# Performance work log

Measured on AMD Instinct MI355X. Metric: run time of the kernel, lower is better.

Reference implementation:

```python
import jax, jax.numpy as jnp
import numpy as np

N = 50000   # nodes
E = 800000  # edges
F_IN, H, C, G = 128, 96, 16, 128  # features, hidden, classes, graphs


def gelu(x):
    return jax.nn.gelu(x, approximate=False)  # torch F.gelu default (erf)


def gcn_conv(x, W, b, src, dst, dis):
    # PyG GCNConv improved=True: A_hat = A + 2I, out = D^-1/2 A_hat D^-1/2 (x W) + b
    xw = x @ W                                   # [N, out]
    norm = dis[src] * dis[dst]                   # [E]
    msg = norm[:, None] * xw[src]                # gather + scale
    out = jax.ops.segment_sum(msg, dst, num_segments=N)
    out = out + (2.0 * dis * dis)[:, None] * xw  # self-loop with weight 2
    return out + b


def setup_inputs() -> dict:
    key = jax.random.key(0)
    ks = jax.random.split(key, 12)
    x = jax.random.normal(ks[0], (N, F_IN), dtype=jnp.float32)
    edge_index = jax.random.randint(ks[1], (2, E), 0, N, dtype=jnp.int64)
    batch = jnp.sort(jax.random.randint(ks[2], (N,), 0, G, dtype=jnp.int64))
    s = lambda fan_in: 1.0 / np.sqrt(fan_in)
    W0 = jax.random.uniform(ks[3], (F_IN, H), jnp.float32, -s(F_IN), s(F_IN))
    b0 = jnp.zeros((H,), jnp.float32)
    W1 = jax.random.uniform(ks[4], (H, H), jnp.float32, -s(H), s(H))
    b1 = jnp.zeros((H,), jnp.float32)
    W2 = jax.random.uniform(ks[5], (H, H), jnp.float32, -s(H), s(H))
    b2 = jnp.zeros((H,), jnp.float32)
    Wc1 = jax.random.uniform(ks[6], (2 * H, H), jnp.float32, -s(2 * H), s(2 * H))
    bc1 = jax.random.uniform(ks[7], (H,), jnp.float32, -s(2 * H), s(2 * H))
    Wc2 = jax.random.uniform(ks[8], (H, C), jnp.float32, -s(H), s(H))
    bc2 = jax.random.uniform(ks[9], (C,), jnp.float32, -s(H), s(H))
    return {"x": x, "edge_index": edge_index, "batch": batch,
            "W0": W0, "b0": b0, "W1": W1, "b1": b1, "W2": W2, "b2": b2,
            "Wc1": Wc1, "bc1": bc1, "Wc2": Wc2, "bc2": bc2}


def reference(x, edge_index, batch, W0, b0, W1, b1, W2, b2, Wc1, bc1, Wc2, bc2):
    src, dst = edge_index[0], edge_index[1]
    # degrees including self-loop weight 2 (improved=True)
    deg = jax.ops.segment_sum(jnp.ones((E,), x.dtype), dst, num_segments=N) + 2.0
    dis = jax.lax.rsqrt(deg)
    # layer 0: GCNConv(F_IN -> H)
    h = gcn_conv(x, W0, b0, src, dst, dis)
    # residual GCNConv layers (dropout is identity at inference)
    h = h + gcn_conv(gelu(h), W1, b1, src, dst, dis)
    h = h + gcn_conv(gelu(h), W2, b2, src, dst, dis)
    h = gelu(h)
    # global mean + max pooling per graph
    cnt = jax.ops.segment_sum(jnp.ones((N,), h.dtype), batch, num_segments=G)
    mean_p = jax.ops.segment_sum(h, batch, num_segments=G) / cnt[:, None]
    max_p = jax.ops.segment_max(h, batch, num_segments=G)
    p = jnp.concatenate([mean_p, max_p], axis=1)  # [G, 2H]
    p = p @ Wc1 + bc1
    p = gelu(p)
    return p @ Wc2 + bc2
```

## Files before the change

### kernel.cpp

```cpp
#include <hip/hip_runtime.h>
#include <hip/hip_bf16.h>

#define DEVINL __device__ __forceinline__

constexpr int N = 50000;
constexpr int E = 800000;
constexpr int F_IN = 128;
constexpr int H = 96;
constexpr int C = 16;
constexpr int G = 128;
constexpr int S = 8;
constexpr int ELLW = 64;

constexpr int OFF_W0  = 0;
constexpr int OFF_W1  = OFF_W0 + F_IN * H;
constexpr int OFF_W2  = OFF_W1 + H * H;
constexpr int OFF_WC1 = OFF_W2 + H * H;
constexpr int OFF_WC2 = OFF_WC1 + 2 * H * H;
constexpr int OFF_B0  = OFF_WC2 + H * C;
constexpr int OFF_B1  = OFF_B0 + H;
constexpr int OFF_B2  = OFF_B1 + H;
constexpr int OFF_BC1 = OFF_B2 + H;
constexpr int OFF_BC2 = OFF_BC1 + H;
constexpr int WF_TOT  = OFF_BC2 + C;

constexpr int CVB   = (WF_TOT + 255) / 256;
constexpr int GEMB  = (N + 31) / 32;
constexpr int SCATB = (E / 2 + 127) / 128;

DEVINL float gelu_f(float x) {
    return 0.5f * x * (1.0f + erff(x * 0.70710678118654752440f));
}

DEVINL int detect_eidx_i64(const int* e) {
    int z = 0;
#pragma unroll
    for (int i = 1; i < 16; i += 2) z |= e[i];
    return z == 0;
}
DEVINL int detect_batch_i64(const int* a) {
    int z = 0;
    for (int i = 20001; i < 20032; i += 2) z |= a[i];
    return z == 0;
}
DEVINL int detect_x_f32(const unsigned short* xu) {
    int bad = 0;
    for (int i = 0; i < 128; i += 2) { int ex = (xu[i] >> 7) & 0xFF; if (ex >= 132) bad = 1; }
    return bad;
}

DEVINL unsigned pk(float a, float b) {
    __hip_bfloat16 ha = __float2bfloat16(a), hb = __float2bfloat16(b);
    unsigned short ua = *(unsigned short*)&ha, ub = *(unsigned short*)&hb;
    return (unsigned)ua | ((unsigned)ub << 16);
}
DEVINL float lo16(unsigned u) { return __uint_as_float(u << 16); }
DEVINL float hi16(unsigned u) { return __uint_as_float(u & 0xffff0000u); }

DEVINL float disv(int c) { return rsqrtf((float)c + 2.0f); }

__global__ void k_prep(const void* W0, const void* W1, const void* W2,
                       const void* Wc1, const void* Wc2,
                       const void* b0, const void* b1, const void* b2,
                       const void* bc1, const void* bc2,
                       const void* x, float* __restrict__ wf, int* __restrict__ cnt) {
    int i = blockIdx.x * 256 + threadIdx.x;
    if (i < N) cnt[i] = 0;
    if (i >= WF_TOT) return;
    int f32 = detect_x_f32((const unsigned short*)x);
    const void* src; int j;
    if      (i < OFF_W1)  { src = W0;  j = i - OFF_W0; }
    else if (i < OFF_W2)  { src = W1;  j = i - OFF_W1; }
    else if (i < OFF_WC1) { src = W2;  j = i - OFF_W2; }
    else if (i < OFF_WC2) { src = Wc1; j = i - OFF_WC1; }
    else if (i < OFF_B0)  { src = Wc2; j = i - OFF_WC2; }
    else if (i < OFF_B1)  { src = b0;  j = i - OFF_B0; }
    else if (i < OFF_B2)  { src = b1;  j = i - OFF_B1; }
    else if (i < OFF_BC1) { src = b2;  j = i - OFF_B2; }
    else if (i < OFF_BC2) { src = bc1; j = i - OFF_BC1; }
    else                  { src = bc2; j = i - OFF_BC2; }
    wf[i] = f32 ? ((const float*)src)[j]
                : __bfloat162float(((const __hip_bfloat16*)src)[j]);
}

template<int K, int KC, bool RAW_IN, bool GELU_IN, bool SCALE_OUT>
DEVINL void gemm_tile(const void* __restrict__ inp, const float* __restrict__ Wf,
                      const int* __restrict__ cnt,
                      int xf32, unsigned* __restrict__ out, int bid, int t) {
    constexpr int R = 32;
    constexpr int NC = K / KC;
    __shared__ __align__(16) float xs[KC][R + 4];
    __shared__ __align__(16) float wsh[KC * 96];
    const int r0 = bid * R;
    const int ty = t >> 4;
    const int tx = t & 15;

    float acc[4][6];
#pragma unroll
    for (int i = 0; i < 4; ++i)
#pragma unroll
        for (int j = 0; j < 6; ++j) acc[i][j] = 0.f;

    for (int c = 0; c < NC; ++c) {
        if (c) __syncthreads();
        for (int idx = t * 4; idx < KC * 96; idx += 128 * 4)
            *(float4*)&wsh[idx] = *(const float4*)&Wf[c * KC * 96 + idx];
        if (RAW_IN && !xf32) {
            for (int idx = t; idx < R * KC; idx += 128) {
                int r = idx / KC, kk = idx - r * KC;
                int row = r0 + r, k = c * KC + kk;
                float v = 0.f;
                if (row < N) v = __bfloat162float(((const __hip_bfloat16*)inp)[(size_t)row * K + k]);
                xs[kk][r] = v;
            }
        } else {
            constexpr int KC4 = KC / 4;
            for (int idx = t; idx < R * KC4; idx += 128) {
                int r = idx / KC4, k4 = (idx - r * KC4) * 4;
                int row = r0 + r, k = c * KC + k4;
                float4 v = make_float4(0.f, 0.f, 0.f, 0.f);
                if (row < N) v = *(const float4*)((const float*)inp + (size_t)row * K + k);
                if (GELU_IN) { v.x = gelu_f(v.x); v.y = gelu_f(v.y); v.z = gelu_f(v.z); v.w = gelu_f(v.w); }
                xs[k4 + 0][r] = v.x; xs[k4 + 1][r] = v.y; xs[k4 + 2][r] = v.z; xs[k4 + 3][r] = v.w;
            }
        }
        __syncthreads();

#pragma unroll 4
        for (int kk = 0; kk < KC; ++kk) {
            float4 av = *(const float4*)&xs[kk][ty * 4];
            float2 b0 = *(const float2*)&wsh[kk * 96 + tx * 6];
            float2 b1 = *(const float2*)&wsh[kk * 96 + tx * 6 + 2];
            float2 b2 = *(const float2*)&wsh[kk * 96 + tx * 6 + 4];
            float a[4] = {av.x, av.y, av.z, av.w};
            float b[6] = {b0.x, b0.y, b1.x, b1.y, b2.x, b2.y};
#pragma unroll
            for (int i = 0; i < 4; ++i)
#pragma unroll
                for (int j = 0; j < 6; ++j)
                    acc[i][j] = fmaf(a[i], b[j], acc[i][j]);
        }
    }

#pragma unroll
    for (int i = 0; i < 4; ++i) {
        int row = r0 + ty * 4 + i;
        if (row < N) {
            float d = SCALE_OUT ? disv(cnt[row]) : 1.0f;
            unsigned* o = out + (size_t)row * 48 + tx * 3;
            o[0] = pk(d * acc[i][0], d * acc[i][1]);
            o[1] = pk(d * acc[i][2], d * acc[i][3]);
            o[2] = pk(d * acc[i][4], d * acc[i][5]);
        }
    }
}

__global__ __launch_bounds__(128) void k_sg(const void* __restrict__ x,
                                            const float* __restrict__ Wf,
                                            const int* __restrict__ eidx,
                                            int* __restrict__ cnt, int* __restrict__ ell,
                                            unsigned* __restrict__ outZ) {
    int b = blockIdx.x, t = threadIdx.x;
    if (b % 3 == 0) {
        int gb = b / 3;
        if (gb >= GEMB) return;
        int xf32 = detect_x_f32((const unsigned short*)x);
        gemm_tile<F_IN, 32, true, false, false>(x, Wf, nullptr, xf32, outZ, gb, t);
        return;
    }
    int sb = (b / 3) * 2 + (b % 3) - 1;
    if (sb >= SCATB) return;
    int t2 = sb * 128 + t;
    int e = 2 * t2;
    if (e >= E) return;
    int i64 = detect_eidx_i64(eidx);
    int s0, s1, d0, d1;
    if (i64) {
        int4 sp = *(const int4*)(eidx + 4 * t2);
        int4 dp = *(const int4*)(eidx + 2 * E + 4 * t2);
        s0 = sp.x; s1 = sp.z; d0 = dp.x; d1 = dp.z;
    } else {
        int2 sp = *(const int2*)(eidx + 2 * t2);
        int2 dp = *(const int2*)(eidx + E + 2 * t2);
        s0 = sp.x; s1 = sp.y; d0 = dp.x; d1 = dp.y;
    }
    int p0 = atomicAdd(&cnt[d0], 1);
    if (p0 < ELLW) ell[d0 * ELLW + p0] = s0;
    if (e + 1 < E) {
        int p1 = atomicAdd(&cnt[d1], 1);
        if (p1 < ELLW) ell[d1 * ELLW + p1] = s1;
    }
}

template<int K, int KC, bool GELU_IN>
__global__ __launch_bounds__(128) void k_gemm(const float* __restrict__ inp,
                                              const float* __restrict__ Wf,
                                              const int* __restrict__ cnt,
                                              unsigned* __restrict__ out) {
    gemm_tile<K, KC, false, GELU_IN, true>(inp, Wf, cnt, 1, out, blockIdx.x, threadIdx.x);
}

template<bool PRESCALED>
__global__ __launch_bounds__(256) void k_aggr(const unsigned* __restrict__ xw, const float* res,
                                              const int* __restrict__ ell, const int* __restrict__ cnt,
                                              const float* __restrict__ bias, float* __restrict__ out) {
    __shared__ int   sIdx[4][ELLW];
    __shared__ float sW[4][ELLW];
    int wid = threadIdx.x >> 6, lane = threadIdx.x & 63;
    int n = blockIdx.x * 4 + wid;
    if (n >= N) return;
    int cn = cnt[n];
    int cc = min(cn, ELLW);
    if (lane < cc) {
        int idx = ell[n * ELLW + lane];
        sIdx[wid][lane] = idx;
        if (!PRESCALED) sW[wid][lane] = disv(cnt[idx]);
    }
    int slot = lane / 12;
    int li = lane - slot * 12;
    int cp = li * 4;
    float4 A0 = make_float4(0.f, 0.f, 0.f, 0.f);
    float4 A1 = make_float4(0.f, 0.f, 0.f, 0.f);
    int j = (slot < 5) ? slot : cc;
    for (; j + 10 < cc; j += 15) {
        int s0 = sIdx[wid][j];
        int s1 = sIdx[wid][j + 5];
        int s2 = sIdx[wid][j + 10];
        uint4 u0 = *(const uint4*)(xw + (size_t)s0 * 48 + cp);
        uint4 u1 = *(const uint4*)(xw + (size_t)s1 * 48 + cp);
        uint4 u2 = *(const uint4*)(xw + (size_t)s2 * 48 + cp);
        if (PRESCALED) {
            A0.x += lo16(u0.x) + lo16(u1.x) + lo16(u2.x);
            A0.y += hi16(u0.x) + hi16(u1.x) + hi16(u2.x);
            A0.z += lo16(u0.y) + lo16(u1.y) + lo16(u2.y);
            A0.w += hi16(u0.y) + hi16(u1.y) + hi16(u2.y);
            A1.x += lo16(u0.z) + lo16(u1.z) + lo16(u2.z);
            A1.y += hi16(u0.z) + hi16(u1.z) + hi16(u2.z);
            A1.z += lo16(u0.w) + lo16(u1.w) + lo16(u2.w);
            A1.w += hi16(u0.w) + hi16(u1.w) + hi16(u2.w);
        } else {
            float w0 = sW[wid][j];
            float w1 = sW[wid][j + 5];
            float w2 = sW[wid][j + 10];
            A0.x = fmaf(w0, lo16(u0.x), A0.x); A0.y = fmaf(w0, hi16(u0.x), A0.y);
            A0.z = fmaf(w0, lo16(u0.y), A0.z); A0.w = fmaf(w0, hi16(u0.y), A0.w);
            A1.x = fmaf(w0, lo16(u0.z), A1.x); A1.y = fmaf(w0, hi16(u0.z), A1.y);
            A1.z = fmaf(w0, lo16(u0.w), A1.z); A1.w = fmaf(w0, hi16(u0.w), A1.w);
            A0.x = fmaf(w1, lo16(u1.x), A0.x); A0.y = fmaf(w1, hi16(u1.x), A0.y);
            A0.z = fmaf(w1, lo16(u1.y), A0.z); A0.w = fmaf(w1, hi16(u1.y), A0.w);
            A1.x = fmaf(w1, lo16(u1.z), A1.x); A1.y = fmaf(w1, hi16(u1.z), A1.y);
            A1.z = fmaf(w1, lo16(u1.w), A1.z); A1.w = fmaf(w1, hi16(u1.w), A1.w);
            A0.x = fmaf(w2, lo16(u2.x), A0.x); A0.y = fmaf(w2, hi16(u2.x), A0.y);
            A0.z = fmaf(w2, lo16(u2.y), A0.z); A0.w = fmaf(w2, hi16(u2.y), A0.w);
            A1.x = fmaf(w2, lo16(u2.z), A1.x); A1.y = fmaf(w2, hi16(u2.z), A1.y);
            A1.z = fmaf(w2, lo16(u2.w), A1.z); A1.w = fmaf(w2, hi16(u2.w), A1.w);
        }
    }
    for (; j < cc; j += 5) {
        int s = sIdx[wid][j];
        uint4 u = *(const uint4*)(xw + (size_t)s * 48 + cp);
        if (PRESCALED) {
            A0.x += lo16(u.x); A0.y += hi16(u.x); A0.z += lo16(u.y); A0.w += hi16(u.y);
            A1.x += lo16(u.z); A1.y += hi16(u.z); A1.z += lo16(u.w); A1.w += hi16(u.w);
        } else {
            float w = sW[wid][j];
            A0.x = fmaf(w, lo16(u.x), A0.x); A0.y = fmaf(w, hi16(u.x), A0.y);
            A0.z = fmaf(w, lo16(u.y), A0.z); A0.w = fmaf(w, hi16(u.y), A0.w);
            A1.x = fmaf(w, lo16(u.z), A1.x); A1.y = fmaf(w, hi16(u.z), A1.y);
            A1.z = fmaf(w, lo16(u.w), A1.z); A1.w = fmaf(w, hi16(u.w), A1.w);
        }
    }
    {
        float g0, g1, g2, g3;
        g0 = __shfl(A0.x, lane + 12); g1 = __shfl(A0.x, lane + 24); g2 = __shfl(A0.x, lane + 36); g3 = __shfl(A0.x, lane + 48);
        A0.x += g0 + g1 + g2 + g3;
        g0 = __shfl(A0.y, lane + 12); g1 = __shfl(A0.y, lane + 24); g2 = __shfl(A0.y, lane + 36); g3 = __shfl(A0.y, lane + 48);
        A0.y += g0 + g1 + g2 + g3;
        g0 = __shfl(A0.z, lane + 12); g1 = __shfl(A0.z, lane + 24); g2 = __shfl(A0.z, lane + 36); g3 = __shfl(A0.z, lane + 48);
        A0.z += g0 + g1 + g2 + g3;
        g0 = __shfl(A0.w, lane + 12); g1 = __shfl(A0.w, lane + 24); g2 = __shfl(A0.w, lane + 36); g3 = __shfl(A0.w, lane + 48);
        A0.w += g0 + g1 + g2 + g3;
        g0 = __shfl(A1.x, lane + 12); g1 = __shfl(A1.x, lane + 24); g2 = __shfl(A1.x, lane + 36); g3 = __shfl(A1.x, lane + 48);
        A1.x += g0 + g1 + g2 + g3;
        g0 = __shfl(A1.y, lane + 12); g1 = __shfl(A1.y, lane + 24); g2 = __shfl(A1.y, lane + 36); g3 = __shfl(A1.y, lane + 48);
        A1.y += g0 + g1 + g2 + g3;
        g0 = __shfl(A1.z, lane + 12); g1 = __shfl(A1.z, lane + 24); g2 = __shfl(A1.z, lane + 36); g3 = __shfl(A1.z, lane + 48);
        A1.z += g0 + g1 + g2 + g3;
        g0 = __shfl(A1.w, lane + 12); g1 = __shfl(A1.w, lane + 24); g2 = __shfl(A1.w, lane + 36); g3 = __shfl(A1.w, lane + 48);
        A1.w += g0 + g1 + g2 + g3;
    }

    if (lane < 12) {
        float dn = disv(cn);
        float sc = PRESCALED ? (2.f * dn) : (2.f * dn * dn);
        int cl = li * 8;
        uint4 su = *(const uint4*)(xw + (size_t)n * 48 + cp);
        float4 sv0 = make_float4(lo16(su.x), hi16(su.x), lo16(su.y), hi16(su.y));
        float4 sv1 = make_float4(lo16(su.z), hi16(su.z), lo16(su.w), hi16(su.w));
        float4 bv0 = *(const float4*)(bias + cl);
        float4 bv1 = *(const float4*)(bias + cl + 4);
        float4 rv0 = make_float4(0.f, 0.f, 0.f, 0.f);
        float4 rv1 = make_float4(0.f, 0.f, 0.f, 0.f);
        if (res) {
            rv0 = *(const float4*)(res + (size_t)n * 96 + cl);
            rv1 = *(const float4*)(res + (size_t)n * 96 + cl + 4);
        }
        float4 o0, o1;
        o0.x = rv0.x + dn * A0.x + sc * sv0.x + bv0.x;
        o0.y = rv0.y + dn * A0.y + sc * sv0.y + bv0.y;
        o0.z = rv0.z + dn * A0.z + sc * sv0.z + bv0.z;
        o0.w = rv0.w + dn * A0.w + sc * sv0.w + bv0.w;
        o1.x = rv1.x + dn * A1.x + sc * sv1.x + bv1.x;
        o1.y = rv1.y + dn * A1.y + sc * sv1.y + bv1.y;
        o1.z = rv1.z + dn * A1.z + sc * sv1.z + bv1.z;
        o1.w = rv1.w + dn * A1.w + sc * sv1.w + bv1.w;
        *(float4*)(out + (size_t)n * 96 + cl) = o0;
        *(float4*)(out + (size_t)n * 96 + cl + 4) = o1;
    }
}

DEVINL int ld_idx(const int* a, int i64, int i) { return i64 ? a[2 * i] : a[i]; }

DEVINL int lbound_s(const int* a, int i64, int n, int key) {
    int lo = 0, hi = n;
    while (lo < hi) { int m = (lo + hi) >> 1; if (ld_idx(a, i64, m) < key) lo = m + 1; else hi = m; }
    return lo;
}

__global__ __launch_bounds__(128) void k_pool(const float* __restrict__ h, const int* __restrict__ batch,
                                              float* __restrict__ part) {
    int i64 = detect_batch_i64(batch);
    int g = blockIdx.x / S, sch = blockIdx.x % S;
    int lo = lbound_s(batch, i64, N, g), hi = lbound_s(batch, i64, N, g + 1);
    int len = hi - lo;
    int a = lo + (int)(((long long)len * sch) / S);
    int b = lo + (int)(((long long)len * (sch + 1)) / S);
    int t = threadIdx.x;
    if (t < 96) {
        float s0 = 0.f, s1 = 0.f, m0 = -INFINITY, m1 = -INFINITY;
        int n = a;
        for (; n + 1 < b; n += 2) {
            float v0 = gelu_f(h[(size_t)n * 96 + t]);
            float v1 = gelu_f(h[(size_t)(n + 1) * 96 + t]);
            s0 += v0; s1 += v1;
            m0 = fmaxf(m0, v0); m1 = fmaxf(m1, v1);
        }
        if (n < b) {
            float v = gelu_f(h[(size_t)n * 96 + t]);
            s0 += v; m0 = fmaxf(m0, v);
        }
        part[(size_t)blockIdx.x * 192 + t] = s0 + s1;
        part[(size_t)blockIdx.x * 192 + 96 + t] = fmaxf(m0, m1);
    }
}

__global__ __launch_bounds__(128) void k_cls(const float* __restrict__ part, const int* __restrict__ batch,
                                             const void* __restrict__ x,
                                             const float* __restrict__ wf, void* __restrict__ outp) {
    __shared__ float p[192];
    __shared__ float q[96];
    int i64 = detect_batch_i64(batch);
    int g = blockIdx.x, t = threadIdx.x;
    int lo = lbound_s(batch, i64, N, g), hi = lbound_s(batch, i64, N, g + 1);
    float inv = (hi > lo) ? 1.f / (float)(hi - lo) : 0.f;
    if (t < 96) {
        float sum = 0.f, mx = -INFINITY;
        for (int s = 0; s < S; ++s) {
            sum += part[(size_t)(g * S + s) * 192 + t];
            mx = fmaxf(mx, part[(size_t)(g * S + s) * 192 + 96 + t]);
        }
        p[t] = sum * inv;
        p[96 + t] = mx;
    }
    __syncthreads();
    if (t < 96) {
        float acc = wf[OFF_BC1 + t];
        const float* Wc1 = wf + OFF_WC1;
        for (int j = 0; j < 192; ++j)
            acc += p[j] * Wc1[j * 96 + t];
        q[t] = gelu_f(acc);
    }
    __syncthreads();
    if (t < 16) {
        float acc = wf[OFF_BC2 + t];
        const float* Wc2 = wf + OFF_WC2;
        for (int j = 0; j < 96; ++j)
            acc += q[j] * Wc2[j * 16 + t];
        if (detect_x_f32((const unsigned short*)x)) ((float*)outp)[g * 16 + t] = acc;
        else ((__hip_bfloat16*)outp)[g * 16 + t] = __float2bfloat16(acc);
    }
}

extern "C" void kernel_launch(void* const* d_in, const int* in_sizes, int n_in,
                              void* d_out, int out_size, void* d_ws, size_t ws_size,
                              hipStream_t stream) {
    const void* x    = d_in[0];
    const int* eidx  = (const int*)d_in[1];
    const int* batch = (const int*)d_in[2];
    (void)in_sizes; (void)n_in; (void)out_size; (void)ws_size;

    char* w = (char*)d_ws;
    size_t off = 0;
    auto take = [&](size_t bytes) { size_t o = off; off += (bytes + 511) & ~(size_t)511; return o; };
    int*      cnt  = (int*)     (w + take((size_t)N * 4));
    float*    wf   = (float*)   (w + take((size_t)WF_TOT * 4));
    int*      ell  = (int*)     (w + take((size_t)N * ELLW * 4));
    unsigned* bufA = (unsigned*)(w + take((size_t)N * 48 * 4));
    float*    bufH = (float*)   (w + take((size_t)N * 96 * 4));
    float*    part = (float*)   (w + take((size_t)G * S * 192 * 4));

    k_prep<<<CVB, 256, 0, stream>>>(d_in[3], d_in[5], d_in[7], d_in[9], d_in[11],
                                    d_in[4], d_in[6], d_in[8], d_in[10], d_in[12],
                                    x, wf, cnt);
    k_sg<<<3 * GEMB, 128, 0, stream>>>(x, wf + OFF_W0, eidx, cnt, ell, bufA);

    int aggr_grid = (N + 3) / 4;
    k_aggr<false><<<aggr_grid, 256, 0, stream>>>(bufA, nullptr, ell, cnt, wf + OFF_B0, bufH);
    k_gemm<H, 48, true><<<GEMB, 128, 0, stream>>>(bufH, wf + OFF_W1, cnt, bufA);
    k_aggr<true><<<aggr_grid, 256, 0, stream>>>(bufA, bufH, ell, cnt, wf + OFF_B1, bufH);
    k_gemm<H, 48, true><<<GEMB, 128, 0, stream>>>(bufH, wf + OFF_W2, cnt, bufA);
    k_aggr<true><<<aggr_grid, 256, 0, stream>>>(bufA, bufH, ell, cnt, wf + OFF_B2, bufH);

    k_pool<<<G * S, 128, 0, stream>>>(bufH, batch, part);
    k_cls<<<G, 128, 0, stream>>>(part, batch, x, wf, d_out);
}
```

Measured before the change: 354.7 us.

## Fuse next-layer GELU+GEMM into aggregation kernel epilogue

The separate GEMM kernels are removed. Each aggregation block now handles 32 nodes and, in its epilogue, applies GELU to the new hidden rows, multiplies them by the next layer's 96x96 weight held in shared memory, and writes the prescaled bf16 features. This drops two kernel launches and the re-read of the hidden buffer from global memory. In exchange every block reloads the 36KB weight matrix, shared memory per block rises (occupancy may drop), and double-buffered xw arrays are needed so a layer does not overwrite its own gather source.

```diff
diff --git a/kernel.cpp b/kernel.cpp
--- a/kernel.cpp
+++ b/kernel.cpp
@@ -27,6 +27,7 @@
 constexpr int CVB   = (WF_TOT + 255) / 256;
 constexpr int GEMB  = (N + 31) / 32;
 constexpr int SCATB = (E / 2 + 127) / 128;
+constexpr int AGB   = (N + 31) / 32;
 
 DEVINL float gelu_f(float x) {
     return 0.5f * x * (1.0f + erff(x * 0.70710678118654752440f));
@@ -192,130 +193,172 @@
     }
 }
 
-template<int K, int KC, bool GELU_IN>
-__global__ __launch_bounds__(128) void k_gemm(const float* __restrict__ inp,
-                                              const float* __restrict__ Wf,
-                                              const int* __restrict__ cnt,
-                                              unsigned* __restrict__ out) {
-    gemm_tile<K, KC, false, GELU_IN, true>(inp, Wf, cnt, 1, out, blockIdx.x, threadIdx.x);
-}
-
-template<bool PRESCALED>
-__global__ __launch_bounds__(256) void k_aggr(const unsigned* __restrict__ xw, const float* res,
-                                              const int* __restrict__ ell, const int* __restrict__ cnt,
-                                              const float* __restrict__ bias, float* __restrict__ out) {
-    __shared__ int   sIdx[4][ELLW];
-    __shared__ float sW[4][ELLW];
-    int wid = threadIdx.x >> 6, lane = threadIdx.x & 63;
-    int n = blockIdx.x * 4 + wid;
-    if (n >= N) return;
-    int cn = cnt[n];
-    int cc = min(cn, ELLW);
-    if (lane < cc) {
-        int idx = ell[n * ELLW + lane];
-        sIdx[wid][lane] = idx;
-        if (!PRESCALED) sW[wid][lane] = disv(cnt[idx]);
-    }
+template<bool PRESCALED, bool EPI>
+__global__ __launch_bounds__(512) void k_ag(const unsigned* __restrict__ xw, const float* res,
+                                            const int* __restrict__ ell, const int* __restrict__ cnt,
+                                            const float* __restrict__ bias,
+                                            const float* __restrict__ Wepi,
+                                            float* __restrict__ outH,
+                                            unsigned* __restrict__ outA) {
+    __shared__ int   sIdx[8][ELLW];
+    __shared__ float sW[8][ELLW];
+    __shared__ float hs[EPI ? 32 : 1][97];
+    __shared__ __align__(16) float wsh[EPI ? 96 * 96 : 4];
+    int t = threadIdx.x;
+    int wv = t >> 6, lane = t & 63;
+    int bn0 = blockIdx.x * 32;
+
+    if (EPI) {
+        for (int idx = t * 4; idx < 96 * 96; idx += 512 * 4)
+            *(float4*)&wsh[idx] = *(const float4*)&Wepi[idx];
+    }
+
     int slot = lane / 12;
     int li = lane - slot * 12;
     int cp = li * 4;
-    float4 A0 = make_float4(0.f, 0.f, 0.f, 0.f);
-    float4 A1 = make_float4(0.f, 0.f, 0.f, 0.f);
-    int j = (slot < 5) ? slot : cc;
-    for (; j + 10 < cc; j += 15) {
-        int s0 = sIdx[wid][j];
-        int s1 = sIdx[wid][j + 5];
-        int s2 = sIdx[wid][j + 10];
-        uint4 u0 = *(const uint4*)(xw + (size_t)s0 * 48 + cp);
-        uint4 u1 = *(const uint4*)(xw + (size_t)s1 * 48 + cp);
-        uint4 u2 = *(const uint4*)(xw + (size_t)s2 * 48 + cp);
-        if (PRESCALED) {
-            A0.x += lo16(u0.x) + lo16(u1.x) + lo16(u2.x);
-            A0.y += hi16(u0.x) + hi16(u1.x) + hi16(u2.x);
-            A0.z += lo16(u0.y) + lo16(u1.y) + lo16(u2.y);
-            A0.w += hi16(u0.y) + hi16(u1.y) + hi16(u2.y);
-            A1.x += lo16(u0.z) + lo16(u1.z) + lo16(u2.z);
-            A1.y += hi16(u0.z) + hi16(u1.z) + hi16(u2.z);
-            A1.z += lo16(u0.w) + lo16(u1.w) + lo16(u2.w);
-            A1.w += hi16(u0.w) + hi16(u1.w) + hi16(u2.w);
-        } else {
-            float w0 = sW[wid][j];
-            float w1 = sW[wid][j + 5];
-            float w2 = sW[wid][j + 10];
-            A0.x = fmaf(w0, lo16(u0.x), A0.x); A0.y = fmaf(w0, hi16(u0.x), A0.y);
-            A0.z = fmaf(w0, lo16(u0.y), A0.z); A0.w = fmaf(w0, hi16(u0.y), A0.w);
-            A1.x = fmaf(w0, lo16(u0.z), A1.x); A1.y = fmaf(w0, hi16(u0.z), A1.y);
-            A1.z = fmaf(w0, lo16(u0.w), A1.z); A1.w = fmaf(w0, hi16(u0.w), A1.w);
-            A0.x = fmaf(w1, lo16(u1.x), A0.x); A0.y = fmaf(w1, hi16(u1.x), A0.y);
-            A0.z = fmaf(w1, lo16(u1.y), A0.z); A0.w = fmaf(w1, hi16(u1.y), A0.w);
-            A1.x = fmaf(w1, lo16(u1.z), A1.x); A1.y = fmaf(w1, hi16(u1.z), A1.y);
-            A1.z = fmaf(w1, lo16(u1.w), A1.z); A1.w = fmaf(w1, hi16(u1.w), A1.w);
-            A0.x = fmaf(w2, lo16(u2.x), A0.x); A0.y = fmaf(w2, hi16(u2.x), A0.y);
-            A0.z = fmaf(w2, lo16(u2.y), A0.z); A0.w = fmaf(w2, hi16(u2.y), A0.w);
-            A1.x = fmaf(w2, lo16(u2.z), A1.x); A1.y = fmaf(w2, hi16(u2.z), A1.y);
-            A1.z = fmaf(w2, lo16(u2.w), A1.z); A1.w = fmaf(w2, hi16(u2.w), A1.w);
-        }
-    }
-    for (; j < cc; j += 5) {
-        int s = sIdx[wid][j];
-        uint4 u = *(const uint4*)(xw + (size_t)s * 48 + cp);
-        if (PRESCALED) {
-            A0.x += lo16(u.x); A0.y += hi16(u.x); A0.z += lo16(u.y); A0.w += hi16(u.y);
-            A1.x += lo16(u.z); A1.y += hi16(u.z); A1.z += lo16(u.w); A1.w += hi16(u.w);
-        } else {
-            float w = sW[wid][j];
-            A0.x = fmaf(w, lo16(u.x), A0.x); A0.y = fmaf(w, hi16(u.x), A0.y);
-            A0.z = fmaf(w, lo16(u.y), A0.z); A0.w = fmaf(w, hi16(u.y), A0.w);
-            A1.x = fmaf(w, lo16(u.z), A1.x); A1.y = fmaf(w, hi16(u.z), A1.y);
-            A1.z = fmaf(w, lo16(u.w), A1.z); A1.w = fmaf(w, hi16(u.w), A1.w);
-        }
-    }
-    {
-        float g0, g1, g2, g3;
-        g0 = __shfl(A0.x, lane + 12); g1 = __shfl(A0.x, lane + 24); g2 = __shfl(A0.x, lane + 36); g3 = __shfl(A0.x, lane + 48);
-        A0.x += g0 + g1 + g2 + g3;
-        g0 = __shfl(A0.y, lane + 12); g1 = __shfl(A0.y, lane + 24); g2 = __shfl(A0.y, lane + 36); g3 = __shfl(A0.y, lane + 48);
-        A0.y += g0 + g1 + g2 + g3;
-        g0 = __shfl(A0.z, lane + 12); g1 = __shfl(A0.z, lane + 24); g2 = __shfl(A0.z, lane + 36); g3 = __shfl(A0.z, lane + 48);
-        A0.z += g0 + g1 + g2 + g3;
-        g0 = __shfl(A0.w, lane + 12); g1 = __shfl(A0.w, lane + 24); g2 = __shfl(A0.w, lane + 36); g3 = __shfl(A0.w, lane + 48);
-        A0.w += g0 + g1 + g2 + g3;
-        g0 = __shfl(A1.x, lane + 12); g1 = __shfl(A1.x, lane + 24); g2 = __shfl(A1.x, lane + 36); g3 = __shfl(A1.x, lane + 48);
-        A1.x += g0 + g1 + g2 + g3;
-        g0 = __shfl(A1.y, lane + 12); g1 = __shfl(A1.y, lane + 24); g2 = __shfl(A1.y, lane + 36); g3 = __shfl(A1.y, lane + 48);
-        A1.y += g0 + g1 + g2 + g3;
-        g0 = __shfl(A1.z, lane + 12); g1 = __shfl(A1.z, lane + 24); g2 = __shfl(A1.z, lane + 36); g3 = __shfl(A1.z, lane + 48);
-        A1.z += g0 + g1 + g2 + g3;
-        g0 = __shfl(A1.w, lane + 12); g1 = __shfl(A1.w, lane + 24); g2 = __shfl(A1.w, lane + 36); g3 = __shfl(A1.w, lane + 48);
-        A1.w += g0 + g1 + g2 + g3;
-    }
-
-    if (lane < 12) {
-        float dn = disv(cn);
-        float sc = PRESCALED ? (2.f * dn) : (2.f * dn * dn);
-        int cl = li * 8;
-        uint4 su = *(const uint4*)(xw + (size_t)n * 48 + cp);
-        float4 sv0 = make_float4(lo16(su.x), hi16(su.x), lo16(su.y), hi16(su.y));
-        float4 sv1 = make_float4(lo16(su.z), hi16(su.z), lo16(su.w), hi16(su.w));
-        float4 bv0 = *(const float4*)(bias + cl);
-        float4 bv1 = *(const float4*)(bias + cl + 4);
-        float4 rv0 = make_float4(0.f, 0.f, 0.f, 0.f);
-        float4 rv1 = make_float4(0.f, 0.f, 0.f, 0.f);
-        if (res) {
-            rv0 = *(const float4*)(res + (size_t)n * 96 + cl);
-            rv1 = *(const float4*)(res + (size_t)n * 96 + cl + 4);
-        }
-        float4 o0, o1;
-        o0.x = rv0.x + dn * A0.x + sc * sv0.x + bv0.x;
-        o0.y = rv0.y + dn * A0.y + sc * sv0.y + bv0.y;
-        o0.z = rv0.z + dn * A0.z + sc * sv0.z + bv0.z;
-        o0.w = rv0.w + dn * A0.w + sc * sv0.w + bv0.w;
-        o1.x = rv1.x + dn * A1.x + sc * sv1.x + bv1.x;
-        o1.y = rv1.y + dn * A1.y + sc * sv1.y + bv1.y;
-        o1.z = rv1.z + dn * A1.z + sc * sv1.z + bv1.z;
-        o1.w = rv1.w + dn * A1.w + sc * sv1.w + bv1.w;
-        *(float4*)(out + (size_t)n * 96 + cl) = o0;
-        *(float4*)(out + (size_t)n * 96 + cl + 4) = o1;
+    int cl = li * 8;
+
+    for (int k = 0; k < 4; ++k) {
+        int r = wv * 4 + k;
+        int n = bn0 + r;
+        if (n >= N) {
+            if (EPI && lane < 12)
+#pragma unroll
+                for (int q = 0; q < 8; ++q) hs[r][cl + q] = 0.f;
+            continue;
+        }
+        int cn = cnt[n];
+        int cc = min(cn, ELLW);
+        if (lane < cc) {
+            int idx = ell[n * ELLW + lane];
+            sIdx[wv][lane] = idx;
+            if (!PRESCALED) sW[wv][lane] = disv(cnt[idx]);
+        }
+        float4 A0 = make_float4(0.f, 0.f, 0.f, 0.f);
+        float4 A1 = make_float4(0.f, 0.f, 0.f, 0.f);
+        int j = (slot < 5) ? slot : cc;
+        for (; j + 10 < cc; j += 15) {
+            int s0 = sIdx[wv][j];
+            int s1 = sIdx[wv][j + 5];
+            int s2 = sIdx[wv][j + 10];
+            uint4 u0 = *(const uint4*)(xw + (size_t)s0 * 48 + cp);
+            uint4 u1 = *(const uint4*)(xw + (size_t)s1 * 48 + cp);
+            uint4 u2 = *(const uint4*)(xw + (size_t)s2 * 48 + cp);
+            if (PRESCALED) {
+                A0.x += lo16(u0.x) + lo16(u1.x) + lo16(u2.x);
+                A0.y += hi16(u0.x) + hi16(u1.x) + hi16(u2.x);
+                A0.z += lo16(u0.y) + lo16(u1.y) + lo16(u2.y);
+                A0.w += hi16(u0.y) + hi16(u1.y) + hi16(u2.y);
+                A1.x += lo16(u0.z) + lo16(u1.z) + lo16(u2.z);
+                A1.y += hi16(u0.z) + hi16(u1.z) + hi16(u2.z);
+                A1.z += lo16(u0.w) + lo16(u1.w) + lo16(u2.w);
+                A1.w += hi16(u0.w) + hi16(u1.w) + hi16(u2.w);
+            } else {
+                float w0 = sW[wv][j];
+                float w1 = sW[wv][j + 5];
+                float w2 = sW[wv][j + 10];
+                A0.x = fmaf(w0, lo16(u0.x), A0.x); A0.y = fmaf(w0, hi16(u0.x), A0.y);
+                A0.z = fmaf(w0, lo16(u0.y), A0.z); A0.w = fmaf(w0, hi16(u0.y), A0.w);
+                A1.x = fmaf(w0, lo16(u0.z), A1.x); A1.y = fmaf(w0, hi16(u0.z), A1.y);
+                A1.z = fmaf(w0, lo16(u0.w), A1.z); A1.w = fmaf(w0, hi16(u0.w), A1.w);
+                A0.x = fmaf(w1, lo16(u1.x), A0.x); A0.y = fmaf(w1, hi16(u1.x), A0.y);
+                A0.z = fmaf(w1, lo16(u1.y), A0.z); A0.w = fmaf(w1, hi16(u1.y), A0.w);
+                A1.x = fmaf(w1, lo16(u1.z), A1.x); A1.y = fmaf(w1, hi16(u1.z), A1.y);
+                A1.z = fmaf(w1, lo16(u1.w), A1.z); A1.w = fmaf(w1, hi16(u1.w), A1.w);
+                A0.x = fmaf(w2, lo16(u2.x), A0.x); A0.y = fmaf(w2, hi16(u2.x), A0.y);
+                A0.z = fmaf(w2, lo16(u2.y), A0.z); A0.w = fmaf(w2, hi16(u2.y), A0.w);
+                A1.x = fmaf(w2, lo16(u2.z), A1.x); A1.y = fmaf(w2, hi16(u2.z), A1.y);
+                A1.z = fmaf(w2, lo16(u2.w), A1.z); A1.w = fmaf(w2, hi16(u2.w), A1.w);
+            }
+        }
+        for (; j < cc; j += 5) {
+            int s = sIdx[wv][j];
+            uint4 u = *(const uint4*)(xw + (size_t)s * 48 + cp);
+            if (PRESCALED) {
+                A0.x += lo16(u.x); A0.y += hi16(u.x); A0.z += lo16(u.y); A0.w += hi16(u.y);
+                A1.x += lo16(u.z); A1.y += hi16(u.z); A1.z += lo16(u.w); A1.w += hi16(u.w);
+            } else {
+                float w = sW[wv][j];
+                A0.x = fmaf(w, lo16(u.x), A0.x); A0.y = fmaf(w, hi16(u.x), A0.y);
+                A0.z = fmaf(w, lo16(u.y), A0.z); A0.w = fmaf(w, hi16(u.y), A0.w);
+                A1.x = fmaf(w, lo16(u.z), A1.x); A1.y = fmaf(w, hi16(u.z), A1.y);
+                A1.z = fmaf(w, lo16(u.w), A1.z); A1.w = fmaf(w, hi16(u.w), A1.w);
+            }
+        }
+        {
+            float g0, g1, g2, g3;
+            g0 = __shfl(A0.x, lane + 12); g1 = __shfl(A0.x, lane + 24); g2 = __shfl(A0.x, lane + 36); g3 = __shfl(A0.x, lane + 48);
+            A0.x += g0 + g1 + g2 + g3;
+            g0 = __shfl(A0.y, lane + 12); g1 = __shfl(A0.y, lane + 24); g2 = __shfl(A0.y, lane + 36); g3 = __shfl(A0.y, lane + 48);
+            A0.y += g0 + g1 + g2 + g3;
+            g0 = __shfl(A0.z, lane + 12); g1 = __shfl(A0.z, lane + 24); g2 = __shfl(A0.z, lane + 36); g3 = __shfl(A0.z, lane + 48);
+            A0.z += g0 + g1 + g2 + g3;
+            g0 = __shfl(A0.w, lane + 12); g1 = __shfl(A0.w, lane + 24); g2 = __shfl(A0.w, lane + 36); g3 = __shfl(A0.w, lane + 48);
+            A0.w += g0 + g1 + g2 + g3;
+            g0 = __shfl(A1.x, lane + 12); g1 = __shfl(A1.x, lane + 24); g2 = __shfl(A1.x, lane + 36); g3 = __shfl(A1.x, lane + 48);
+            A1.x += g0 + g1 + g2 + g3;
+            g0 = __shfl(A1.y, lane + 12); g1 = __shfl(A1.y, lane + 24); g2 = __shfl(A1.y, lane + 36); g3 = __shfl(A1.y, lane + 48);
+            A1.y += g0 + g1 + g2 + g3;
+            g0 = __shfl(A1.z, lane + 12); g1 = __shfl(A1.z, lane + 24); g2 = __shfl(A1.z, lane + 36); g3 = __shfl(A1.z, lane + 48);
+            A1.z += g0 + g1 + g2 + g3;
+            g0 = __shfl(A1.w, lane + 12); g1 = __shfl(A1.w, lane + 24); g2 = __shfl(A1.w, lane + 36); g3 = __shfl(A1.w, lane + 48);
+            A1.w += g0 + g1 + g2 + g3;
+        }
+
+        if (lane < 12) {
+            float dn = disv(cn);
+            float sc = PRESCALED ? (2.f * dn) : (2.f * dn * dn);
+            uint4 su = *(const uint4*)(xw + (size_t)n * 48 + cp);
+            float4 sv0 = make_float4(lo16(su.x), hi16(su.x), lo16(su.y), hi16(su.y));
+            float4 sv1 = make_float4(lo16(su.z), hi16(su.z), lo16(su.w), hi16(su.w));
+            float4 bv0 = *(const float4*)(bias + cl);
+            float4 bv1 = *(const float4*)(bias + cl + 4);
+            float4 rv0 = make_float4(0.f, 0.f, 0.f, 0.f);
+            float4 rv1 = make_float4(0.f, 0.f, 0.f, 0.f);
+            if (res) {
+                rv0 = *(const float4*)(res + (size_t)n * 96 + cl);
+                rv1 = *(const float4*)(res + (size_t)n * 96 + cl + 4);
+            }
+            float4 o0, o1;
+            o0.x = rv0.x + dn * A0.x + sc * sv0.x + bv0.x;
+            o0.y = rv0.y + dn * A0.y + sc * sv0.y + bv0.y;
+            o0.z = rv0.z + dn * A0.z + sc * sv0.z + bv0.z;
+            o0.w = rv0.w + dn * A0.w + sc * sv0.w + bv0.w;
+            o1.x = rv1.x + dn * A1.x + sc * sv1.x + bv1.x;
+            o1.y = rv1.y + dn * A1.y + sc * sv1.y + bv1.y;
+            o1.z = rv1.z + dn * A1.z + sc * sv1.z + bv1.z;
+            o1.w = rv1.w + dn * A1.w + sc * sv1.w + bv1.w;
+            *(float4*)(outH + (size_t)n * 96 + cl) = o0;
+            *(float4*)(outH + (size_t)n * 96 + cl + 4) = o1;
+            if (EPI) {
+                hs[r][cl + 0] = gelu_f(o0.x); hs[r][cl + 1] = gelu_f(o0.y);
+                hs[r][cl + 2] = gelu_f(o0.z); hs[r][cl + 3] = gelu_f(o0.w);
+                hs[r][cl + 4] = gelu_f(o1.x); hs[r][cl + 5] = gelu_f(o1.y);
+                hs[r][cl + 6] = gelu_f(o1.z); hs[r][cl + 7] = gelu_f(o1.w);
+            }
+        }
+    }
+    if (!EPI) return;
+    __syncthreads();
+    int ty = t >> 4, tx = t & 15;
+    float acc[6] = {0.f, 0.f, 0.f, 0.f, 0.f, 0.f};
+#pragma unroll 4
+    for (int kk = 0; kk < 96; ++kk) {
+        float a = hs[ty][kk];
+        float2 b0 = *(const float2*)&wsh[kk * 96 + tx * 6];
+        float2 b1 = *(const float2*)&wsh[kk * 96 + tx * 6 + 2];
+        float2 b2 = *(const float2*)&wsh[kk * 96 + tx * 6 + 4];
+        acc[0] = fmaf(a, b0.x, acc[0]); acc[1] = fmaf(a, b0.y, acc[1]);
+        acc[2] = fmaf(a, b1.x, acc[2]); acc[3] = fmaf(a, b1.y, acc[3]);
+        acc[4] = fmaf(a, b2.x, acc[4]); acc[5] = fmaf(a, b2.y, acc[5]);
+    }
+    int row = bn0 + ty;
+    if (row < N) {
+        float d = disv(cnt[row]);
+        unsigned* o = outA + (size_t)row * 48 + tx * 3;
+        o[0] = pk(d * acc[0], d * acc[1]);
+        o[1] = pk(d * acc[2], d * acc[3]);
+        o[2] = pk(d * acc[4], d * acc[5]);
     }
 }
 
@@ -402,24 +445,25 @@
     char* w = (char*)d_ws;
     size_t off = 0;
     auto take = [&](size_t bytes) { size_t o = off; off += (bytes + 511) & ~(size_t)511; return o; };
-    int*      cnt  = (int*)     (w + take((size_t)N * 4));
-    float*    wf   = (float*)   (w + take((size_t)WF_TOT * 4));
-    int*      ell  = (int*)     (w + take((size_t)N * ELLW * 4));
-    unsigned* bufA = (unsigned*)(w + take((size_t)N * 48 * 4));
-    float*    bufH = (float*)   (w + take((size_t)N * 96 * 4));
-    float*    part = (float*)   (w + take((size_t)G * S * 192 * 4));
+    int*      cnt   = (int*)     (w + take((size_t)N * 4));
+    float*    wf    = (float*)   (w + take((size_t)WF_TOT * 4));
+    int*      ell   = (int*)     (w + take((size_t)N * ELLW * 4));
+    unsigned* bufA0 = (unsigned*)(w + take((size_t)N * 48 * 4));
+    unsigned* bufA1 = (unsigned*)(w + take((size_t)N * 48 * 4));
+    float*    bufH  = (float*)   (w + take((size_t)N * 96 * 4));
+    float*    part  = (float*)   (w + take((size_t)G * S * 192 * 4));
 
     k_prep<<<CVB, 256, 0, stream>>>(d_in[3], d_in[5], d_in[7], d_in[9], d_in[11],
                                     d_in[4], d_in[6], d_in[8], d_in[10], d_in[12],
                                     x, wf, cnt);
-    k_sg<<<3 * GEMB, 128, 0, stream>>>(x, wf + OFF_W0, eidx, cnt, ell, bufA);
-
-    int aggr_grid = (N + 3) / 4;
-    k_aggr<false><<<aggr_grid, 256, 0, stream>>>(bufA, nullptr, ell, cnt, wf + OFF_B0, bufH);
-    k_gemm<H, 48, true><<<GEMB, 128, 0, stream>>>(bufH, wf + OFF_W1, cnt, bufA);
-    k_aggr<true><<<aggr_grid, 256, 0, stream>>>(bufA, bufH, ell, cnt, wf + OFF_B1, bufH);
-    k_gemm<H, 48, true><<<GEMB, 128, 0, stream>>>(bufH, wf + OFF_W2, cnt, bufA);
-    k_aggr<true><<<aggr_grid, 256, 0, stream>>>(bufA, bufH, ell, cnt, wf + OFF_B2, bufH);
+    k_sg<<<3 * GEMB, 128, 0, stream>>>(x, wf + OFF_W0, eidx, cnt, ell, bufA0);
+
+    k_ag<false, true><<<AGB, 512, 0, stream>>>(bufA0, nullptr, ell, cnt, wf + OFF_B0,
+                                               wf + OFF_W1, bufH, bufA1);
+    k_ag<true, true><<<AGB, 512, 0, stream>>>(bufA1, bufH, ell, cnt, wf + OFF_B1,
+                                              wf + OFF_W2, bufH, bufA0);
+    k_ag<true, false><<<AGB, 512, 0, stream>>>(bufA0, bufH, ell, cnt, wf + OFF_B2,
+                                               nullptr, bufH, nullptr);
 
     k_pool<<<G * S, 128, 0, stream>>>(bufH, batch, part);
     k_cls<<<G, 128, 0, stream>>>(part, batch, x, wf, d_out);
```

Measured after the change: 413.0 us. +16.4%, slower.
